# Kernel optimization log

Measured on AMD Instinct MI355X. Metric: run time of the kernel, lower is better.

## Reference

```python
import jax, jax.numpy as jnp
import numpy as np

B, F_IN, N, S = 2, 128, 192, 192   # batch, in_features, n_nodes, seq (seq==n_nodes required by mask broadcast)
H, D = 4, 64                        # n_heads, n_hidden (out_features = H*D = 256)
NEG_SLOPE = 0.2


def setup_inputs() -> dict:
    key = jax.random.key(0)
    ks = jax.random.split(key, 6)
    X = jax.random.normal(ks[0], (B, F_IN, N, S), dtype=jnp.float32)
    A = jax.random.randint(ks[1], (N, N, 1), 0, 2, dtype=jnp.int32)
    W_lin = jax.random.normal(ks[2], (F_IN, H * D), dtype=jnp.float32) * 0.05
    b_lin = jax.random.uniform(ks[3], (H * D,), dtype=jnp.float32)
    W_attn = jax.random.normal(ks[4], (2 * D,), dtype=jnp.float32) * 0.05
    b_attn = jax.random.uniform(ks[5], (1,), dtype=jnp.float32)
    return {"X": X, "A": A, "W_lin": W_lin, "b_lin": b_lin,
            "W_attn": W_attn, "b_attn": b_attn}


def reference(X, A, W_lin, b_lin, W_attn, b_attn):
    # Dropout is identity (eval mode).
    b, f, n, s = X.shape
    x = jnp.transpose(X, (0, 3, 2, 1))                      # (b, s, n, f)
    g = (x @ W_lin + b_lin).reshape(b, s, n, H, D)          # (b, s, n, H, D)
    # attn is affine: attn(cat[g_i, g_j]) = a_src.g_i + a_dst.g_j + b_attn
    a_src, a_dst = W_attn[:D], W_attn[D:]
    s_src = jnp.einsum('bsnhd,d->bsnh', g, a_src)
    s_dst = jnp.einsum('bsnhd,d->bsnh', g, a_dst)
    e = s_src[:, :, :, None, :] + s_dst[:, :, None, :, :] + b_attn[0]  # (b, s, n_i, n_j, H)
    e = jnp.where(e >= 0, e, NEG_SLOPE * e)                 # LeakyReLU
    # torch masked_fill broadcast: mask (n,n,1,1) aligns with e dims (s, n_i, n_j, H)
    e = jnp.where(A[..., None] == 0, -jnp.inf, e)
    alphas = jax.nn.softmax(e, axis=1)                      # softmax over seq dim (dim=1, as in source)
    alphas = jnp.nan_to_num(alphas, nan=0.0)
    # einsum 'mnojh,klphf->mnohf': independent sums over j (alphas) and k,l,p (g)
    sum_g = g.sum(axis=(0, 1, 2))                           # (H, D)
    attn_res = alphas.sum(axis=3)[..., None] * sum_g        # (b, s, n, H, D)
    out = attn_res.reshape(b, s, n, H * D)                  # concat=True
    return jnp.transpose(out, (0, 3, 2, 1))                 # (b, out_features, n, s)
```

## Files before the change

kernel.cpp:

```cpp
#include <hip/hip_runtime.h>
#include <math.h>

#define B_ 2
#define F_ 128
#define N_ 192
#define S_ 192
#define NS_ (N_ * S_)
#define SLOPE 0.2f
#define LOG2E 1.4426950408889634f
#define NEG_INF (-__builtin_inff())

#if defined(__has_builtin)
#if __has_builtin(__builtin_amdgcn_exp2f)
#define EXP2(x) __builtin_amdgcn_exp2f(x)
#else
#define EXP2(x) exp2f(x)
#endif
#else
#define EXP2(x) exp2f(x)
#endif

__device__ __forceinline__ float lrelu(float e) { return fmaxf(e, SLOPE * e); }

#define OFF_WSRC 0
#define OFF_WDST 512
#define OFF_CSRC 1024
#define OFF_CDST 1028
#define OFF_SUMG 1040
#define OFF_XSUM 1296
#define OFF_SRC  1552
#define OFF_DST2 (OFF_SRC + 8 * NS_)
#define OFF_DST1 (OFF_DST2 + 8 * NS_)

__global__ __launch_bounds__(256) void k1(const float* __restrict__ X,
                                          const float* __restrict__ W_lin,
                                          const float* __restrict__ b_lin,
                                          const float* __restrict__ W_attn,
                                          const float* __restrict__ b_attn,
                                          float* __restrict__ ws) {
    int blk = blockIdx.x, t = threadIdx.x;
    if (blk < 256) {
        int f = blk & 127, b = blk >> 7;
        const float4* p = (const float4*)(X + ((size_t)b * F_ + f) * NS_);
        float acc = 0.f;
        for (int i = t; i < NS_ / 4; i += 256) {
            float4 v = p[i];
            acc += (v.x + v.y) + (v.z + v.w);
        }
        for (int o = 32; o; o >>= 1) acc += __shfl_down(acc, o, 64);
        __shared__ float red[4];
        if ((t & 63) == 0) red[t >> 6] = acc;
        __syncthreads();
        if (t == 0) ws[OFF_XSUM + b * 128 + f] = (red[0] + red[1]) + (red[2] + red[3]);
    } else if (blk == 256) {
        const float4* wa = (const float4*)W_attn;
        for (int c = t; c < 512; c += 256) {
            int f = c >> 2, h = c & 3;
            const float4* wl = (const float4*)(W_lin + f * 256 + h * 64);
            float as = 0.f, ad = 0.f;
#pragma unroll
            for (int q = 0; q < 16; q++) {
                float4 w = wl[q], a1 = wa[q], a2 = wa[16 + q];
                as += w.x * a1.x + w.y * a1.y + w.z * a1.z + w.w * a1.w;
                ad += w.x * a2.x + w.y * a2.y + w.z * a2.z + w.w * a2.w;
            }
            ws[OFF_WSRC + c] = as * LOG2E;
            ws[OFF_WDST + c] = ad * LOG2E;
        }
    } else {
        if (t < 4) {
            float c = 0.f;
            for (int d = 0; d < 64; d++) c += b_lin[t * 64 + d] * W_attn[d];
            ws[OFF_CSRC + t] = (c + b_attn[0]) * LOG2E;
        } else if (t < 8) {
            int h = t - 4;
            float c = 0.f;
            for (int d = 0; d < 64; d++) c += b_lin[h * 64 + d] * W_attn[64 + d];
            ws[OFF_CDST + h] = c * LOG2E;
        }
    }
}

__global__ __launch_bounds__(512) void k2(const float* __restrict__ X,
                                          const int* __restrict__ A,
                                          const float* __restrict__ W_lin,
                                          const float* __restrict__ b_lin,
                                          float* __restrict__ ws) {
    __shared__ float4 wsl[128], wdl[128];
    __shared__ __align__(16) float red[192 * 65];
    int t = threadIdx.x;
    int blk = blockIdx.x;
    if (blk < 384) {
        int n = blk % 192, b = blk / 192;
        if (t < 128) {
            wsl[t] = ((const float4*)(ws + OFF_WSRC))[t];
            wdl[t] = ((const float4*)(ws + OFF_WDST))[t];
        }
        __syncthreads();
        int fq = t >> 6, lane = t & 63;
        float aS[4][3] = {{0}}, aD[4][3] = {{0}};
        const float* xp = X + (size_t)(b * F_) * NS_ + n * S_ + lane;
        int f0 = fq * 16;
#pragma unroll 4
        for (int fi = 0; fi < 16; fi++) {
            const float* xf = xp + (size_t)(f0 + fi) * NS_;
            float x0 = xf[0], x1 = xf[64], x2 = xf[128];
            float4 w1 = wsl[f0 + fi], w2 = wdl[f0 + fi];
            aS[0][0] += x0 * w1.x; aS[0][1] += x1 * w1.x; aS[0][2] += x2 * w1.x;
            aS[1][0] += x0 * w1.y; aS[1][1] += x1 * w1.y; aS[1][2] += x2 * w1.y;
            aS[2][0] += x0 * w1.z; aS[2][1] += x1 * w1.z; aS[2][2] += x2 * w1.z;
            aS[3][0] += x0 * w1.w; aS[3][1] += x1 * w1.w; aS[3][2] += x2 * w1.w;
            aD[0][0] += x0 * w2.x; aD[0][1] += x1 * w2.x; aD[0][2] += x2 * w2.x;
            aD[1][0] += x0 * w2.y; aD[1][1] += x1 * w2.y; aD[1][2] += x2 * w2.y;
            aD[2][0] += x0 * w2.z; aD[2][1] += x1 * w2.z; aD[2][2] += x2 * w2.z;
            aD[3][0] += x0 * w2.w; aD[3][1] += x1 * w2.w; aD[3][2] += x2 * w2.w;
        }
#pragma unroll
        for (int h = 0; h < 4; h++)
#pragma unroll
            for (int k = 0; k < 3; k++) {
                int s = lane + 64 * k;
                red[s * 65 + fq * 8 + h] = aS[h][k];
                red[s * 65 + fq * 8 + 4 + h] = aD[h][k];
            }
        __syncthreads();
        if (t < 192) {
            int s = t;
            bool masked = (A[s * 192 + n] == 0);
#pragma unroll
            for (int h = 0; h < 4; h++) {
                float vS = 0.f, vD = 0.f;
#pragma unroll
                for (int q = 0; q < 8; q++) {
                    vS += red[s * 65 + q * 8 + h];
                    vD += red[s * 65 + q * 8 + 4 + h];
                }
                float sv = vS + ws[OFF_CSRC + h];
                float dv = vD + ws[OFF_CDST + h];
                int bh = b * 4 + h;
                ws[OFF_SRC + bh * NS_ + n * 192 + s] = masked ? NEG_INF : sv;
                ws[OFF_DST2 + bh * NS_ + n * 192 + s] = dv;
                ws[OFF_DST1 + bh * NS_ + s * 192 + n] = dv;
            }
        }
    } else {
        float* xs = (float*)wsl;
        if (t < 128) xs[t] = ws[OFF_XSUM + t] + ws[OFF_XSUM + 128 + t];
        __syncthreads();
        float acc = 0.f;
        for (int ch = 0; ch < 8; ch++) {
            const float4* s4 = (const float4*)(W_lin + ch * 4096);
            ((float4*)red)[t] = s4[t];
            ((float4*)red)[512 + t] = s4[512 + t];
            __syncthreads();
            if (t < 256) {
#pragma unroll
                for (int fi = 0; fi < 16; fi++)
                    acc += xs[ch * 16 + fi] * red[fi * 256 + t];
            }
            __syncthreads();
        }
        if (t < 256) ws[OFF_SUMG + t] = acc + 73728.f * b_lin[t];
    }
}

__global__ __launch_bounds__(768) void k3(const float* __restrict__ ws,
                                          float* __restrict__ out) {
    int iq = blockIdx.x, bh = blockIdx.y;
    int t = threadIdx.x;
    __shared__ float p_sh[768];
    __shared__ float zpart[4 * 768];
    __shared__ float zr_sh[768];
    __shared__ float sg_sh[64];
    const float* src = ws + OFF_SRC + bh * NS_;
    const float* d1 = ws + OFF_DST1 + bh * NS_;
    const float* d2 = ws + OFF_DST2 + bh * NS_;
    int h = bh & 3;
    if (t < 64) sg_sh[t] = ws[OFF_SUMG + h * 64 + t];
    p_sh[t] = src[iq * 768 + t];
    __syncthreads();

    {
        int sq = t / 192, j = t - sq * 192;
        float z0 = 0, z1 = 0, z2 = 0, z3 = 0;
        const float* d1p = d1 + j;
#pragma unroll 4
        for (int s = sq * 48; s < sq * 48 + 48; s++) {
            float q = d1p[s * 192];
            z0 += EXP2(lrelu(p_sh[s] + q));
            z1 += EXP2(lrelu(p_sh[192 + s] + q));
            z2 += EXP2(lrelu(p_sh[384 + s] + q));
            z3 += EXP2(lrelu(p_sh[576 + s] + q));
        }
        float* zp = zpart + sq * 768 + j;
        zp[0] = z0; zp[192] = z1; zp[384] = z2; zp[576] = z3;
    }
    __syncthreads();
    {
        float Z = zpart[t] + zpart[768 + t] + zpart[1536 + t] + zpart[2304 + t];
        zr_sh[t] = (Z != 0.f) ? (1.f / Z) : 0.f;
    }
    __syncthreads();

    {
        int i_loc = t / 192, s = t - i_loc * 192;
        float pv = p_sh[t];
        const float* zr = zr_sh + i_loc * 192;
        float acc = 0.f;
#pragma unroll 4
        for (int j = 0; j < 192; j++) {
            float q = d2[j * 192 + s];
            acc += EXP2(lrelu(pv + q)) * zr[j];
        }
        int b = bh >> 2;
        int i = iq * 4 + i_loc;
        float* op = out + (((size_t)(b * 256 + h * 64)) * 192 + i) * 192 + s;
#pragma unroll 8
        for (int d = 0; d < 64; d++)
            op[(size_t)d * NS_] = acc * sg_sh[d];
    }
}

extern "C" void kernel_launch(void* const* d_in, const int* in_sizes, int n_in,
                              void* d_out, int out_size, void* d_ws, size_t ws_size,
                              hipStream_t stream) {
    const float* X      = (const float*)d_in[0];
    const int*   A      = (const int*)d_in[1];
    const float* W_lin  = (const float*)d_in[2];
    const float* b_lin  = (const float*)d_in[3];
    const float* W_attn = (const float*)d_in[4];
    const float* b_attn = (const float*)d_in[5];
    float* out = (float*)d_out;
    float* ws  = (float*)d_ws;

    k1<<<258, 256, 0, stream>>>(X, W_lin, b_lin, W_attn, b_attn, ws);
    k2<<<385, 512, 0, stream>>>(X, A, W_lin, b_lin, ws);
    k3<<<dim3(48, 8), 768, 0, stream>>>(ws, out);
}
```

Measured before the change: 167.5 us.

## Split all three kernels into more, smaller blocks for better CU occupancy

The X column-sum kernel now splits each (b,f) plane into four quarter-blocks that write partial sums. The projection kernel splits the seq dimension into three 64-wide chunks with 256-thread blocks instead of 512, so each block does less work and uses much less LDS. The attention kernel handles 2 query rows per block with 384 threads instead of 4 rows with 768, giving 768 blocks instead of 384. The aim is to fill the 256 CUs more evenly; the cost is more redundant loads of the softmax denominators, since the d1 column sweep is repeated by twice as many blocks.

```diff
diff --git a/kernel.cpp b/kernel.cpp
--- a/kernel.cpp
+++ b/kernel.cpp
@@ -27,32 +27,34 @@
 #define OFF_CSRC 1024
 #define OFF_CDST 1028
 #define OFF_SUMG 1040
-#define OFF_XSUM 1296
-#define OFF_SRC  1552
+#define OFF_PART 1296
+#define OFF_SRC  2320
 #define OFF_DST2 (OFF_SRC + 8 * NS_)
 #define OFF_DST1 (OFF_DST2 + 8 * NS_)
 
-__global__ __launch_bounds__(256) void k1(const float* __restrict__ X,
-                                          const float* __restrict__ W_lin,
-                                          const float* __restrict__ b_lin,
-                                          const float* __restrict__ W_attn,
-                                          const float* __restrict__ b_attn,
-                                          float* __restrict__ ws) {
+__global__ __launch_bounds__(256) void kPre(const float* __restrict__ X,
+                                            const float* __restrict__ W_lin,
+                                            const float* __restrict__ b_lin,
+                                            const float* __restrict__ W_attn,
+                                            const float* __restrict__ b_attn,
+                                            float* __restrict__ ws) {
     int blk = blockIdx.x, t = threadIdx.x;
-    if (blk < 256) {
-        int f = blk & 127, b = blk >> 7;
-        const float4* p = (const float4*)(X + ((size_t)b * F_ + f) * NS_);
+    if (blk < 1024) {
+        int sq = blk & 3, f = (blk >> 2) & 127, b = blk >> 9;
+        const float4* p = (const float4*)(X + ((size_t)(b * F_ + f)) * NS_ + sq * 9216);
         float acc = 0.f;
-        for (int i = t; i < NS_ / 4; i += 256) {
-            float4 v = p[i];
+#pragma unroll
+        for (int k = 0; k < 9; k++) {
+            float4 v = p[t + k * 256];
             acc += (v.x + v.y) + (v.z + v.w);
         }
         for (int o = 32; o; o >>= 1) acc += __shfl_down(acc, o, 64);
         __shared__ float red[4];
         if ((t & 63) == 0) red[t >> 6] = acc;
         __syncthreads();
-        if (t == 0) ws[OFF_XSUM + b * 128 + f] = (red[0] + red[1]) + (red[2] + red[3]);
-    } else if (blk == 256) {
+        if (t == 0)
+            ws[OFF_PART + sq * 256 + b * 128 + f] = (red[0] + red[1]) + (red[2] + red[3]);
+    } else if (blk == 1024) {
         const float4* wa = (const float4*)W_attn;
         for (int c = t; c < 512; c += 256) {
             int f = c >> 2, h = c & 3;
@@ -81,123 +83,111 @@
     }
 }
 
-__global__ __launch_bounds__(512) void k2(const float* __restrict__ X,
-                                          const int* __restrict__ A,
-                                          const float* __restrict__ W_lin,
-                                          const float* __restrict__ b_lin,
-                                          float* __restrict__ ws) {
+__global__ __launch_bounds__(256) void kProj(const float* __restrict__ X,
+                                             const int* __restrict__ A,
+                                             const float* __restrict__ W_lin,
+                                             const float* __restrict__ b_lin,
+                                             float* __restrict__ ws) {
     __shared__ float4 wsl[128], wdl[128];
-    __shared__ __align__(16) float red[192 * 65];
-    int t = threadIdx.x;
-    int blk = blockIdx.x;
-    if (blk < 384) {
-        int n = blk % 192, b = blk / 192;
+    __shared__ float red[4 * 64 * 9];
+    __shared__ float xs[128];
+    __shared__ float wbuf[4096];
+    int t = threadIdx.x, blk = blockIdx.x;
+    if (blk < 1152) {
+        int n = blk % 192, bsc = blk / 192;
+        int b = bsc / 3, sc = bsc % 3;
         if (t < 128) {
             wsl[t] = ((const float4*)(ws + OFF_WSRC))[t];
             wdl[t] = ((const float4*)(ws + OFF_WDST))[t];
         }
         __syncthreads();
         int fq = t >> 6, lane = t & 63;
-        float aS[4][3] = {{0}}, aD[4][3] = {{0}};
-        const float* xp = X + (size_t)(b * F_) * NS_ + n * S_ + lane;
-        int f0 = fq * 16;
-#pragma unroll 4
-        for (int fi = 0; fi < 16; fi++) {
-            const float* xf = xp + (size_t)(f0 + fi) * NS_;
-            float x0 = xf[0], x1 = xf[64], x2 = xf[128];
+        int s = sc * 64 + lane;
+        float aS[4] = {0, 0, 0, 0}, aD[4] = {0, 0, 0, 0};
+        const float* xp = X + (size_t)(b * F_) * NS_ + n * S_ + s;
+        int f0 = fq * 32;
+#pragma unroll 8
+        for (int fi = 0; fi < 32; fi++) {
+            float x = xp[(size_t)(f0 + fi) * NS_];
             float4 w1 = wsl[f0 + fi], w2 = wdl[f0 + fi];
-            aS[0][0] += x0 * w1.x; aS[0][1] += x1 * w1.x; aS[0][2] += x2 * w1.x;
-            aS[1][0] += x0 * w1.y; aS[1][1] += x1 * w1.y; aS[1][2] += x2 * w1.y;
-            aS[2][0] += x0 * w1.z; aS[2][1] += x1 * w1.z; aS[2][2] += x2 * w1.z;
-            aS[3][0] += x0 * w1.w; aS[3][1] += x1 * w1.w; aS[3][2] += x2 * w1.w;
-            aD[0][0] += x0 * w2.x; aD[0][1] += x1 * w2.x; aD[0][2] += x2 * w2.x;
-            aD[1][0] += x0 * w2.y; aD[1][1] += x1 * w2.y; aD[1][2] += x2 * w2.y;
-            aD[2][0] += x0 * w2.z; aD[2][1] += x1 * w2.z; aD[2][2] += x2 * w2.z;
-            aD[3][0] += x0 * w2.w; aD[3][1] += x1 * w2.w; aD[3][2] += x2 * w2.w;
-        }
-#pragma unroll
-        for (int h = 0; h < 4; h++)
-#pragma unroll
-            for (int k = 0; k < 3; k++) {
-                int s = lane + 64 * k;
-                red[s * 65 + fq * 8 + h] = aS[h][k];
-                red[s * 65 + fq * 8 + 4 + h] = aD[h][k];
+            aS[0] += x * w1.x; aS[1] += x * w1.y; aS[2] += x * w1.z; aS[3] += x * w1.w;
+            aD[0] += x * w2.x; aD[1] += x * w2.y; aD[2] += x * w2.z; aD[3] += x * w2.w;
+        }
+        float* rp = red + t * 9;
+#pragma unroll
+        for (int h = 0; h < 4; h++) { rp[h] = aS[h]; rp[4 + h] = aD[h]; }
+        __syncthreads();
+#pragma unroll
+        for (int c = t; c < 512; c += 256) {
+            int s_loc = c >> 3, k = c & 7;
+            float v = red[s_loc * 9 + k] + red[(64 + s_loc) * 9 + k] +
+                      red[(128 + s_loc) * 9 + k] + red[(192 + s_loc) * 9 + k];
+            int ss = sc * 64 + s_loc;
+            if (k < 4) {
+                int bh = b * 4 + k;
+                bool masked = (A[ss * 192 + n] == 0);
+                ws[OFF_SRC + bh * NS_ + n * 192 + ss] =
+                    masked ? NEG_INF : (v + ws[OFF_CSRC + k]);
+            } else {
+                int h = k - 4, bh = b * 4 + h;
+                float dv = v + ws[OFF_CDST + h];
+                ws[OFF_DST2 + bh * NS_ + n * 192 + ss] = dv;
+                ws[OFF_DST1 + bh * NS_ + ss * 192 + n] = dv;
             }
-        __syncthreads();
-        if (t < 192) {
-            int s = t;
-            bool masked = (A[s * 192 + n] == 0);
-#pragma unroll
-            for (int h = 0; h < 4; h++) {
-                float vS = 0.f, vD = 0.f;
-#pragma unroll
-                for (int q = 0; q < 8; q++) {
-                    vS += red[s * 65 + q * 8 + h];
-                    vD += red[s * 65 + q * 8 + 4 + h];
-                }
-                float sv = vS + ws[OFF_CSRC + h];
-                float dv = vD + ws[OFF_CDST + h];
-                int bh = b * 4 + h;
-                ws[OFF_SRC + bh * NS_ + n * 192 + s] = masked ? NEG_INF : sv;
-                ws[OFF_DST2 + bh * NS_ + n * 192 + s] = dv;
-                ws[OFF_DST1 + bh * NS_ + s * 192 + n] = dv;
-            }
         }
     } else {
-        float* xs = (float*)wsl;
-        if (t < 128) xs[t] = ws[OFF_XSUM + t] + ws[OFF_XSUM + 128 + t];
-        __syncthreads();
+        if (t < 128) {
+            float v = 0.f;
+#pragma unroll
+            for (int q = 0; q < 8; q++) v += ws[OFF_PART + q * 128 + t];
+            xs[t] = v;
+        }
         float acc = 0.f;
         for (int ch = 0; ch < 8; ch++) {
             const float4* s4 = (const float4*)(W_lin + ch * 4096);
-            ((float4*)red)[t] = s4[t];
-            ((float4*)red)[512 + t] = s4[512 + t];
             __syncthreads();
-            if (t < 256) {
-#pragma unroll
-                for (int fi = 0; fi < 16; fi++)
-                    acc += xs[ch * 16 + fi] * red[fi * 256 + t];
-            }
+#pragma unroll
+            for (int k = 0; k < 4; k++) ((float4*)wbuf)[t + k * 256] = s4[t + k * 256];
             __syncthreads();
-        }
-        if (t < 256) ws[OFF_SUMG + t] = acc + 73728.f * b_lin[t];
-    }
-}
-
-__global__ __launch_bounds__(768) void k3(const float* __restrict__ ws,
-                                          float* __restrict__ out) {
-    int iq = blockIdx.x, bh = blockIdx.y;
-    int t = threadIdx.x;
-    __shared__ float p_sh[768];
-    __shared__ float zpart[4 * 768];
-    __shared__ float zr_sh[768];
+#pragma unroll
+            for (int fi = 0; fi < 16; fi++) acc += xs[ch * 16 + fi] * wbuf[fi * 256 + t];
+        }
+        ws[OFF_SUMG + t] = acc + 73728.f * b_lin[t];
+    }
+}
+
+__global__ __launch_bounds__(384) void kAttn(const float* __restrict__ ws,
+                                             float* __restrict__ out) {
+    int blk = blockIdx.x, t = threadIdx.x;
+    int bh = blk & 7, iq = blk >> 3;
+    int b = bh >> 2, h = bh & 3;
+    __shared__ float p_sh[384];
+    __shared__ float zpart[2 * 384];
+    __shared__ float zr_sh[384];
     __shared__ float sg_sh[64];
     const float* src = ws + OFF_SRC + bh * NS_;
     const float* d1 = ws + OFF_DST1 + bh * NS_;
     const float* d2 = ws + OFF_DST2 + bh * NS_;
-    int h = bh & 3;
     if (t < 64) sg_sh[t] = ws[OFF_SUMG + h * 64 + t];
-    p_sh[t] = src[iq * 768 + t];
+    p_sh[t] = src[iq * 384 + t];
     __syncthreads();
 
     {
         int sq = t / 192, j = t - sq * 192;
-        float z0 = 0, z1 = 0, z2 = 0, z3 = 0;
+        float z0 = 0.f, z1 = 0.f;
         const float* d1p = d1 + j;
-#pragma unroll 4
-        for (int s = sq * 48; s < sq * 48 + 48; s++) {
+#pragma unroll 8
+        for (int s = sq * 96; s < sq * 96 + 96; s++) {
             float q = d1p[s * 192];
             z0 += EXP2(lrelu(p_sh[s] + q));
             z1 += EXP2(lrelu(p_sh[192 + s] + q));
-            z2 += EXP2(lrelu(p_sh[384 + s] + q));
-            z3 += EXP2(lrelu(p_sh[576 + s] + q));
-        }
-        float* zp = zpart + sq * 768 + j;
-        zp[0] = z0; zp[192] = z1; zp[384] = z2; zp[576] = z3;
+        }
+        zpart[sq * 384 + j] = z0;
+        zpart[sq * 384 + 192 + j] = z1;
     }
     __syncthreads();
     {
-        float Z = zpart[t] + zpart[768 + t] + zpart[1536 + t] + zpart[2304 + t];
+        float Z = zpart[t] + zpart[384 + t];
         zr_sh[t] = (Z != 0.f) ? (1.f / Z) : 0.f;
     }
     __syncthreads();
@@ -207,13 +197,12 @@
         float pv = p_sh[t];
         const float* zr = zr_sh + i_loc * 192;
         float acc = 0.f;
-#pragma unroll 4
+#pragma unroll 8
         for (int j = 0; j < 192; j++) {
             float q = d2[j * 192 + s];
             acc += EXP2(lrelu(pv + q)) * zr[j];
         }
-        int b = bh >> 2;
-        int i = iq * 4 + i_loc;
+        int i = iq * 2 + i_loc;
         float* op = out + (((size_t)(b * 256 + h * 64)) * 192 + i) * 192 + s;
 #pragma unroll 8
         for (int d = 0; d < 64; d++)
@@ -233,7 +222,7 @@
     float* out = (float*)d_out;
     float* ws  = (float*)d_ws;
 
-    k1<<<258, 256, 0, stream>>>(X, W_lin, b_lin, W_attn, b_attn, ws);
-    k2<<<385, 512, 0, stream>>>(X, A, W_lin, b_lin, ws);
-    k3<<<dim3(48, 8), 768, 0, stream>>>(ws, out);
-}
+    kPre<<<1026, 256, 0, stream>>>(X, W_lin, b_lin, W_attn, b_attn, ws);
+    kProj<<<1153, 256, 0, stream>>>(X, A, W_lin, b_lin, ws);
+    kAttn<<<768, 384, 0, stream>>>(ws, out);
+}
```

New measurement: 150.9 us. 10.0% less time.
